# Kernel tuning notes

Hardware: AMD Instinct MI355X
Metric: run time of the kernel (lower is better)

## Reference

```python
import jax, jax.numpy as jnp
import numpy as np

B, T, C, H, W = 2, 8, 4, 128, 128
P = 8; D = 128; DEPTH = 2; E = 4; HD = 2 * D
Hp, Wp = H // P, W // P; F2 = 2 * D; CPP = C * P * P


def _ln(x, g, b):
    m = x.mean(-1, keepdims=True)
    v = ((x - m) ** 2).mean(-1, keepdims=True)
    return (x - m) * jax.lax.rsqrt(v + 1e-5) * g + b


def setup_inputs():
    key = jax.random.key(0)
    it = iter(jax.random.split(key, 32))
    def n(shape, s=0.02):
        return jax.random.normal(next(it), shape, jnp.float32) * s
    z = lambda shape: jnp.zeros(shape, jnp.float32)
    return {
        "x": jax.random.normal(next(it), (B, T, C, H, W), jnp.float32),
        "dt": jax.random.uniform(next(it), (T,), jnp.float32, 0.1, 1.0),
        "enc_Wre": n((CPP, D)), "enc_Wim": n((CPP, D)),
        "dec_W": n((F2, CPP)), "dec_b": z((CPP,)),
        "ln_sp_g": jnp.ones((DEPTH, F2), jnp.float32), "ln_sp_b": z((DEPTH, F2)),
        "conv_W": n((DEPTH, F2, F2, 3, 3), 0.05), "conv_b": z((DEPTH, F2)),
        "E_re": n((DEPTH, D, D), 0.05), "E_im": n((DEPTH, D, D), 0.05),
        "Dc_re": n((DEPTH, D, D), 0.05), "Dc_im": n((DEPTH, D, D), 0.05),
        "gate_W": n((DEPTH, F2, D)), "gate_b": z((DEPTH, D)),
        "src_W": n((DEPTH, F2, F2)), "src_b": z((DEPTH, F2)),
        "flux_decay": z((DEPTH, D)),
        "lam_re": n((DEPTH, D), 0.5), "lam_im": n((DEPTH, D), 0.5),
        "ln_t_g": jnp.ones((DEPTH, F2), jnp.float32), "ln_t_b": z((DEPTH, F2)),
        "rtr_W": n((DEPTH, F2, E)),
        "W1": n((DEPTH, E, F2, HD)), "b1": z((DEPTH, E, HD)),
        "W2": n((DEPTH, E, HD, F2)), "b2": z((DEPTH, E, F2)),
    }


def _forward(x, dt, enc_Wre, enc_Wim, dec_W, dec_b, ln_sp_g, ln_sp_b, conv_W, conv_b,
             E_re, E_im, Dc_re, Dc_im, gate_W, gate_b, src_W, src_b, flux_decay,
             lam_re, lam_im, ln_t_g, ln_t_b, rtr_W, W1, b1, W2, b2):
    Bx, Tx = x.shape[:2]
    # patch-embed encoder -> complex latent [B,T,D,Hp,Wp]
    f = x.reshape(Bx, Tx, C, Hp, P, Wp, P).transpose(0, 1, 3, 5, 2, 4, 6).reshape(Bx, Tx, Hp, Wp, CPP)
    zc = (f @ enc_Wre) + 1j * (f @ enc_Wim)
    zc = zc.transpose(0, 1, 4, 2, 3)
    dtBT = jnp.broadcast_to(dt[None, :], (Bx, Tx))
    flux = jnp.zeros((Bx, D), jnp.complex64)
    for i in range(DEPTH):
        # spatial branch: LayerNorm over [re,im] channels + Clifford-style 3x3 conv
        zr = jnp.concatenate([zc.real, zc.imag], axis=2).reshape(Bx * Tx, F2, Hp, Wp)
        xn = _ln(zr.transpose(0, 2, 3, 1), ln_sp_g[i], ln_sp_b[i]).transpose(0, 3, 1, 2)
        xs = jax.lax.conv_general_dilated(xn, conv_W[i], (1, 1), 'SAME',
                                          dimension_numbers=('NCHW', 'OIHW', 'NCHW')) + conv_b[i][None, :, None, None]
        sre, sim = jnp.split(xs, 2, axis=1)
        zc = zc + (sre + 1j * sim).reshape(Bx, Tx, D, Hp, Wp)
        # eigen-basis encode (complex channel mixing)
        xe = zc.transpose(0, 1, 3, 4, 2) @ (E_re[i] + 1j * E_im[i])  # B,T,Hp,Wp,D
        xm = xe.mean(axis=(2, 3))  # B,T,D complex
        # sequential flux tracker: inherently recurrent -> lax.scan over T
        gW, gb, sW, sb = gate_W[i], gate_b[i], src_W[i], src_b[i]
        dec = jax.nn.sigmoid(flux_decay[i])
        def step(fl, xmt):
            inp = jnp.concatenate([xmt.real, xmt.imag], -1)
            gate = jax.nn.sigmoid(inp @ gW + gb)
            s2 = inp @ sW + sb
            src = s2[..., :D] + 1j * s2[..., D:]
            fn = dec * fl + gate * xmt + (1.0 - gate) * src
            return fn, (fn, src)
        flux, (flux_seq, src_seq) = jax.lax.scan(step, flux, xm.transpose(1, 0, 2))
        flux_seq = flux_seq.transpose(1, 0, 2)
        src_seq = src_seq.transpose(1, 0, 2)
        g = jax.nn.sigmoid(jnp.concatenate([flux_seq.real, flux_seq.imag], -1) @ gW + gb)[:, :, None, None, :]
        forcing = xe * g + src_seq[:, :, None, None, :] * (1.0 - g)
        # complex transition operators (ZOH-style discretization)
        lam = -jax.nn.softplus(lam_re[i]) + 1j * lam_im[i]  # [D]
        opd = jnp.exp(dtBT[:, :, None] * lam[None, None, :])  # B,T,D complex
        opf = (opd - 1.0) / lam
        u = forcing * opf[:, :, None, None, :]
        A = jnp.broadcast_to(opd[:, :, None, None, :], u.shape)
        def comb(a, b):
            aA, aX = a
            bA, bX = b
            return (aA * bA, bX + bA * aX)
        # parallel pscan over time: h_t = A_t*h_{t-1} + u_t, independent per (B,Hp,Wp)
        _, uo = jax.lax.associative_scan(comb, (A, u), axis=1)
        xo = uo @ (Dc_re[i] + 1j * Dc_im[i])  # basis decode, B,T,Hp,Wp,D
        xon = _ln(jnp.concatenate([xo.real, xo.imag], -1), ln_t_g[i], ln_t_b[i])
        xcc = xon[..., :D] + 1j * xon[..., D:]
        # MoE FFN with soft routing over experts
        ft = jnp.concatenate([xcc.real, xcc.imag], -1).reshape(-1, F2)  # [M,2D]
        gates = jax.nn.softmax(ft @ rtr_W[i], axis=-1)  # [M,E]
        hmid = jax.nn.gelu(jnp.einsum('mf,efh->emh', ft, W1[i]) + b1[i][:, None, :])
        oexp = jnp.einsum('emh,ehf->emf', hmid, W2[i]) + b2[i][:, None, :]
        dtok = jnp.einsum('me,emf->mf', gates, oexp).reshape(Bx, Tx, Hp, Wp, F2)
        delta = dtok[..., :D] + 1j * dtok[..., D:]
        zc = zc + (xcc + delta).transpose(0, 1, 4, 2, 3)
    # decoder: project [re,im] -> pixels and unpatchify (real output)
    zl = zc.transpose(0, 1, 3, 4, 2)
    fo = jnp.concatenate([zl.real, zl.imag], -1) @ dec_W + dec_b
    return fo.reshape(Bx, Tx, Hp, Wp, C, P, P).transpose(0, 1, 4, 2, 5, 3, 6).reshape(Bx, Tx, C, H, W)


def reference(x, dt, enc_Wre, enc_Wim, dec_W, dec_b, ln_sp_g, ln_sp_b, conv_W, conv_b,
              E_re, E_im, Dc_re, Dc_im, gate_W, gate_b, src_W, src_b, flux_decay,
              lam_re, lam_im, ln_t_g, ln_t_b, rtr_W, W1, b1, W2, b2):
    return _forward(x, dt, enc_Wre, enc_Wim, dec_W, dec_b, ln_sp_g, ln_sp_b, conv_W, conv_b,
                    E_re, E_im, Dc_re, Dc_im, gate_W, gate_b, src_W, src_b, flux_decay,
                    lam_re, lam_im, ln_t_g, ln_t_b, rtr_W, W1, b1, W2, b2)
```

## Files before the change

kernel.cpp:

```cpp
#include <hip/hip_runtime.h>
#include <hip/hip_bf16.h>
#include <math.h>


#define NIN 28
typedef unsigned short u16;
typedef __attribute__((ext_vector_type(8))) short bf16x8;
typedef __attribute__((ext_vector_type(4))) float f32x4;
typedef __attribute__((ext_vector_type(8))) unsigned short us8;
typedef __attribute__((ext_vector_type(4))) unsigned short us4;

__device__ __forceinline__ float b2f(u16 u){ union{unsigned i;float f;}v; v.i=((unsigned)u)<<16; return v.f; }
__device__ __forceinline__ u16 f2b(float x){ __hip_bfloat16 h=__float2bfloat16(x); return *(u16*)&h; }
__device__ __forceinline__ float loadraw(const void* p, size_t i, int bf){
  return bf? b2f(((const u16*)p)[i]) : ((const float*)p)[i];
}
__device__ __forceinline__ float d_sigmoid(float x){ return 1.0f/(1.0f+expf(-x)); }
__device__ __forceinline__ float d_softplus(float x){ return fmaxf(x,0.0f)+log1pf(expf(-fabsf(x))); }
__device__ __forceinline__ float d_gelu(float x){
  const float c=0.7978845608028654f;
  return 0.5f*x*(1.0f+tanhf(c*(x+0.044715f*x*x*x)));
}

__global__ void detect_k(const void* lnspg, int* flag){
  unsigned w=*(const unsigned*)lnspg;
  *flag=(w==0x3F803F80u)?1:0;
}

#define NF32 17
struct MP {
  const void* src[NIN];
  int f32dst[NF32]; int f32cum[NF32+1];
  int seg[7];
};

__global__ __launch_bounds__(256) void mega_prep(MP a, const int* __restrict__ flag, float* __restrict__ W,
    u16* __restrict__ encB, u16* __restrict__ decB, u16* __restrict__ convB,
    u16* __restrict__ cplxB, u16* __restrict__ w1B, u16* __restrict__ w2c,
    const int* f32srcIdx_unused){
  int g=blockIdx.x*256+threadIdx.x;
  if(g>=a.seg[6]) return;
  int bf=*flag;
  if(g<a.seg[0]){
    int i=0;
    while(i<NF32-1 && g>=a.f32cum[i+1]) i++;
    int local=g-a.f32cum[i];
    const int needs[NF32]={1,5,6,7,9,14,15,16,17,18,19,20,21,22,23,25,27};
    W[a.f32dst[i]+local]=loadraw(a.src[needs[i]], local, bf);
  } else if(g<a.seg[1]){
    int idx=g-a.seg[0]; int n=idx>>8, k=idx&255;
    float v=(n<128)? loadraw(a.src[2],(size_t)k*128+n,bf) : loadraw(a.src[3],(size_t)k*128+(n-128),bf);
    encB[idx]=f2b(v);
  } else if(g<a.seg[2]){
    int idx=g-a.seg[1]; int n=idx>>8, k=idx&255;
    decB[idx]=f2b(loadraw(a.src[4],(size_t)k*256+n,bf));
  } else if(g<a.seg[3]){
    int idx=g-a.seg[2];
    int i=idx/589824; int r=idx-i*589824;
    int o=r/2304; int k=r-o*2304;
    int kg=k>>8, ic=k&255; int ky=kg/3, kx=kg-3*ky;
    size_t s=((((size_t)i*256+o)*256+ic)*3+ky)*3+kx;
    convB[idx]=f2b(loadraw(a.src[8],s,bf));
  } else if(g<a.seg[4]){
    int idx=g-a.seg[3];
    int mat=idx>>16; int r=idx&65535; int n=r>>8, k=r&255;
    int depth=mat&1; int isD=mat>>1;
    const void* re=isD? a.src[12]:a.src[10];
    const void* im=isD? a.src[13]:a.src[11];
    size_t base=(size_t)depth*16384;
    float v;
    if(k<128){ v = (n<128)? loadraw(re,base+(size_t)k*128+n,bf) : loadraw(im,base+(size_t)k*128+(n-128),bf); }
    else{ int kk=k-128;
      v = (n<128)? -loadraw(im,base+(size_t)kk*128+n,bf) : loadraw(re,base+(size_t)kk*128+(n-128),bf); }
    cplxB[idx]=f2b(v);
  } else if(g<a.seg[5]){
    int idx=g-a.seg[4]; int m=idx>>16; int r=idx&65535; int n=r>>8, k=r&255;
    w1B[idx]=f2b(loadraw(a.src[24],(size_t)m*65536+(size_t)k*256+n,bf));
  } else {
    int idx=g-a.seg[5];
    int i=idx>>18; int r=idx&262143; int n=r>>10; int k=r&1023;
    int e=k>>8, h=k&255;
    size_t s=(((size_t)(i*4+e)*256+h)*256+n);
    w2c[idx]=f2b(loadraw(a.src[26],s,bf));
  }
}

#define FB_BIAS 1
#define FB_GELU 2
#define FB_RS 4
#define FB_ADDTO 8
#define FB_WF32 16
#define FB_WBF16 32
#define FB_CONV 64
#define FB_GATHER 128
#define FB_MOE2 256
#define FB_UNPATCH 512

template<int FLAGS>
__global__ __launch_bounds__(512,2) void mfma_gemm(
    const void* __restrict__ Asrc, const u16* __restrict__ Bt,
    const float* __restrict__ bias, const float* __restrict__ gates,
    float* __restrict__ Cf, u16* __restrict__ Cb,
    const u16* __restrict__ Xtra, void* __restrict__ Cout, const int* __restrict__ flagp,
    int K, long aE, long bE, long biasE, long cE, long cRow)
{
  __shared__ u16 As[64][72];
  __shared__ u16 Bs[64][72];
  const int e=blockIdx.z;
  const u16* A=(const u16*)Asrc + (size_t)e*aE;
  Bt += (size_t)e*bE;
  const float* biasp = bias? bias+(size_t)e*biasE : nullptr;
  const int bn=blockIdx.x*64, bm=blockIdx.y*64;
  const int tid=threadIdx.x, l=tid&63, w=tid>>6;
  const int wm=w&3, wn=w>>2;
  const int row=tid>>3, col8=(tid&7)<<3;
  int bf=0;
  if(FLAGS&(FB_GATHER|FB_UNPATCH)) bf=*flagp;
  const us8 z8={0,0,0,0,0,0,0,0};
  us8 ra, rbv;

  auto loadA=[&](int k0){
    int gk=k0+col8;
    if(FLAGS&FB_CONV){
      int m=bm+row; int bt=m>>8, rem=m&255, hp=rem>>4, wp=rem&15;
      int kg=gk>>8, ic=gk&255; int ky=kg/3, kx=kg-3*ky;
      int y=hp+ky-1, x=wp+kx-1;
      ra = ((unsigned)y<16u && (unsigned)x<16u)?
           *(const us8*)&A[(((size_t)(bt*16+y))*16+x)*256+ic] : z8;
    } else if(FLAGS&FB_GATHER){
      int m=bm+row; int bt=m>>8, rem=m&255, hp=rem>>4, wp=rem&15;
      int c=gk>>6, ph=(gk>>3)&7;
      size_t sidx=(((size_t)bt*4+c)<<14)+(size_t)((hp*8+ph)<<7)+wp*8;
      if(bf) ra=*(const us8*)&((const u16*)Asrc)[sidx];
      else{
        const float* xf=(const float*)Asrc + sidx;
        us8 t;
        #pragma unroll
        for(int j=0;j<8;j++) t[j]=f2b(xf[j]);
        ra=t;
      }
    } else {
      ra=*(const us8*)&A[(size_t)(bm+row)*K+gk];
    }
  };
  auto loadB=[&](int k0){ rbv=*(const us8*)&Bt[(size_t)(bn+row)*K+k0+col8]; };

  loadA(0); loadB(0);
  f32x4 acc0={0.f,0.f,0.f,0.f}, acc1={0.f,0.f,0.f,0.f};
  const int kSteps=K>>6;
  for(int ks=0; ks<kSteps; ++ks){
    __syncthreads();
    *(us8*)&As[row][col8]=ra;
    *(us8*)&Bs[row][col8]=rbv;
    if(ks+1<kSteps){ loadA((ks+1)<<6); loadB((ks+1)<<6); }
    __syncthreads();
    #pragma unroll
    for(int kk=0;kk<64;kk+=32){
      const int kc=kk+((l>>4)<<3);
      bf16x8 a =*(const bf16x8*)&As[wm*16      +(l&15)][kc];
      bf16x8 b0=*(const bf16x8*)&Bs[wn*32      +(l&15)][kc];
      bf16x8 b1=*(const bf16x8*)&Bs[wn*32 + 16 +(l&15)][kc];
      acc0=__builtin_amdgcn_mfma_f32_16x16x32_bf16(a,b0,acc0,0,0,0);
      acc1=__builtin_amdgcn_mfma_f32_16x16x32_bf16(a,b1,acc1,0,0,0);
    }
  }

  const int rr=(l>>4)<<2, cc=l&15;
  #pragma unroll
  for(int ni=0;ni<2;ni++){
    f32x4 av = ni? acc1:acc0;
    #pragma unroll
    for(int r=0;r<4;r++){
      int m=bm+wm*16+rr+r;
      int n=bn+wn*32+ni*16+cc;
      float v=av[r];
      if(FLAGS&FB_BIAS) v+=biasp[n];
      if(FLAGS&FB_GELU) v=d_gelu(v);
      if(FLAGS&FB_RS)   v*=gates[(size_t)m*4+e];
      if(FLAGS&FB_MOE2){
        #pragma unroll
        for(int ee=0;ee<4;ee++) v+=gates[(size_t)m*4+ee]*bias[ee*256+n];
        v+=b2f(Xtra[(size_t)m*256+n]);
      }
      if(FLAGS&FB_UNPATCH){
        int bt=m>>8, hp=(m>>4)&15, wp=m&15;
        int c=n>>6, ph=(n>>3)&7, pw=n&7;
        size_t o=((size_t)bt<<16)|((size_t)c<<14)|((size_t)(hp*8+ph)<<7)|(size_t)(wp*8+pw);
        if(bf) ((__hip_bfloat16*)Cout)[o]=__float2bfloat16(v);
        else   ((float*)Cout)[o]=v;
        continue;
      }
      size_t o=(size_t)e*cE + (size_t)m*cRow + n;
      if(FLAGS&FB_ADDTO) v+=Cf[o];
      if(FLAGS&(FB_WF32|FB_ADDTO)) Cf[o]=v;
      if(FLAGS&FB_WBF16) Cb[o]=f2b(v);
    }
  }
}

__global__ __launch_bounds__(256) void ln4_k(const float* __restrict__ X,
    const float* __restrict__ g, const float* __restrict__ b, u16* __restrict__ out,
    const float* __restrict__ rtr, float* __restrict__ gates){
  int row=blockIdx.x*4+(threadIdx.x>>6);
  int l=threadIdx.x&63;
  f32x4 v=*(const f32x4*)&X[(size_t)row*256+l*4];
  float s=v[0]+v[1]+v[2]+v[3];
  #pragma unroll
  for(int o=32;o;o>>=1) s+=__shfl_xor(s,o);
  float mean=s*(1.0f/256.0f);
  float d0=v[0]-mean,d1=v[1]-mean,d2=v[2]-mean,d3=v[3]-mean;
  float q=d0*d0+d1*d1+d2*d2+d3*d3;
  #pragma unroll
  for(int o=32;o;o>>=1) q+=__shfl_xor(q,o);
  float rs=rsqrtf(q*(1.0f/256.0f)+1e-5f);
  float nv[4]={d0,d1,d2,d3};
  us4 o4;
  #pragma unroll
  for(int j=0;j<4;j++){ nv[j]=nv[j]*rs*g[l*4+j]+b[l*4+j]; o4[j]=f2b(nv[j]); }
  *(us4*)&out[(size_t)row*256+l*4]=o4;
  if(rtr){
    float p[4]={0.f,0.f,0.f,0.f};
    #pragma unroll
    for(int j=0;j<4;j++)
      #pragma unroll
      for(int ee=0;ee<4;ee++) p[ee]+=nv[j]*rtr[(l*4+j)*4+ee];
    #pragma unroll
    for(int ee=0;ee<4;ee++)
      #pragma unroll
      for(int o=32;o;o>>=1) p[ee]+=__shfl_xor(p[ee],o);
    if(l==0){
      float mx=fmaxf(fmaxf(p[0],p[1]),fmaxf(p[2],p[3]));
      float e0=expf(p[0]-mx),e1=expf(p[1]-mx),e2=expf(p[2]-mx),e3=expf(p[3]-mx);
      float inv=1.0f/(e0+e1+e2+e3);
      gates[row*4+0]=e0*inv; gates[row*4+1]=e1*inv; gates[row*4+2]=e2*inv; gates[row*4+3]=e3*inv;
    }
  }
}

__global__ __launch_bounds__(256) void reduce_xm4(const float* __restrict__ xe, float* __restrict__ xm4){
  int bt=blockIdx.x, ch=blockIdx.y, c=threadIdx.x;
  const float* base=xe+((size_t)bt*256+ch*64)*256+c;
  float s=0.f;
  #pragma unroll 4
  for(int sp=0;sp<64;sp++) s+=base[(size_t)sp*256];
  xm4[(bt*4+ch)*256+c]=s;
}

__global__ __launch_bounds__(384) void gate_src_k(const float* __restrict__ xm4,
    const float* __restrict__ sW, const float* __restrict__ sb,
    const float* __restrict__ gW, const float* __restrict__ gb,
    float* __restrict__ xm, float* __restrict__ s2, float* __restrict__ gt,
    const float* __restrict__ dt, const float* __restrict__ lam_re, const float* __restrict__ lam_im,
    float* __restrict__ odr_, float* __restrict__ odi_, float* __restrict__ ofr_, float* __restrict__ ofi_){
  int tid=threadIdx.x;
  if(blockIdx.x==16){
    for(int idx=tid; idx<1024; idx+=384){
      int t=idx>>7, d=idx&127;
      float lr=-d_softplus(lam_re[d]);
      float li=lam_im[d];
      float dtv=dt[t];
      float er=expf(dtv*lr);
      float odr=er*cosf(dtv*li), odi=er*sinf(dtv*li);
      float den=lr*lr+li*li;
      float ar=odr-1.0f, ai=odi;
      odr_[idx]=odr; odi_[idx]=odi;
      ofr_[idx]=(ar*lr+ai*li)/den;
      ofi_[idx]=(ai*lr-ar*li)/den;
    }
    return;
  }
  int bt=blockIdx.x;
  __shared__ float inp[256];
  if(tid<256){
    float v=(xm4[(bt*4+0)*256+tid]+xm4[(bt*4+1)*256+tid]
            +xm4[(bt*4+2)*256+tid]+xm4[(bt*4+3)*256+tid])*(1.0f/256.0f);
    inp[tid]=v; xm[bt*256+tid]=v;
  }
  __syncthreads();
  if(tid<256){
    float acc=sb[tid];
    for(int k=0;k<256;k++) acc+=inp[k]*sW[k*256+tid];
    s2[bt*256+tid]=acc;
  }else{
    int d=tid-256;
    float acc=gb[d];
    for(int k=0;k<256;k++) acc+=inp[k]*gW[k*128+d];
    gt[bt*128+d]=d_sigmoid(acc);
  }
}

__global__ __launch_bounds__(128) void flux_gate2(const float* __restrict__ xm,
    const float* __restrict__ s2, const float* __restrict__ gt,
    const float* __restrict__ fdec, const float* __restrict__ fbin, float* __restrict__ fbout,
    const float* __restrict__ gW, const float* __restrict__ gb, float* __restrict__ gbuf, int init){
  int bt=blockIdx.x; int b=bt>>3, t=bt&7; int d=threadIdx.x;
  float flr = init? 0.f : fbin[b*256+d];
  float fli = init? 0.f : fbin[b*256+128+d];
  float dec = d_sigmoid(fdec[d]);
  for(int tp=0; tp<=t; tp++){
    int q=b*8+tp;
    float gv=gt[q*128+d];
    flr = dec*flr + gv*xm[q*256+d]     + (1.0f-gv)*s2[q*256+d];
    fli = dec*fli + gv*xm[q*256+128+d] + (1.0f-gv)*s2[q*256+128+d];
  }
  __shared__ float inp[256];
  inp[d]=flr; inp[128+d]=fli;
  __syncthreads();
  float acc=gb[d];
  for(int k=0;k<256;k++) acc+=inp[k]*gW[k*128+d];
  gbuf[bt*128+d]=d_sigmoid(acc);
  if(t==7){ fbout[b*256+d]=flr; fbout[b*256+128+d]=fli; }
}

__global__ __launch_bounds__(256) void fscan_t(const float* __restrict__ xe,
    const float* __restrict__ gbuf, const float* __restrict__ ss,
    const float* __restrict__ odr, const float* __restrict__ odi,
    const float* __restrict__ ofr, const float* __restrict__ ofi, u16* __restrict__ uo){
  int idx=blockIdx.x*256+threadIdx.x;
  int d=idx&127, s=(idx>>7)&255, b=idx>>15;
  float hr=0.f, hi=0.f;
  for(int t=0;t<8;t++){
    int bt=b*8+t;
    size_t n=(size_t)bt*256+s;
    float g=gbuf[bt*128+d];
    float sr=ss[bt*256+d], si=ss[bt*256+128+d];
    float xr=xe[n*256+d], xi=xe[n*256+128+d];
    float fr=xr*g+sr*(1.0f-g), fi=xi*g+si*(1.0f-g);
    float pr=ofr[t*128+d], pi=ofi[t*128+d];
    float ur=fr*pr-fi*pi, ui=fr*pi+fi*pr;
    float ar=odr[t*128+d], ai=odi[t*128+d];
    float nr=ar*hr-ai*hi+ur, ni=ar*hi+ai*hr+ui;
    hr=nr; hi=ni;
    uo[n*256+d]=f2b(hr); uo[n*256+128+d]=f2b(hi);
  }
}

extern "C" void kernel_launch(void* const* d_in, const int* in_sizes, int n_in,
                              void* d_out, int out_size, void* d_ws, size_t ws_size,
                              hipStream_t stream){
  (void)out_size; (void)ws_size; (void)n_in;
  int acum[NIN+1]; acum[0]=0;
  for(int i=0;i<NIN;i++) acum[i+1]=acum[i]+((i==0)?0:in_sizes[i]);
  const int totalA=acum[NIN];
  float* W=(float*)d_ws;
  size_t off=((size_t)totalA+63)&~(size_t)63;
  int*   flag=(int*)(W+off); off+=64;
  float* zc  =W+off; off+=1048576;
  float* xe  =W+off; off+=1048576;
  u16* zcb =(u16*)(W+off); off+=524288;
  u16* xnb =(u16*)(W+off); off+=524288;
  u16* uob =(u16*)(W+off); off+=524288;
  u16* ftb =(u16*)(W+off); off+=524288;
  u16* hmid=(u16*)(W+off); off+=2097152;
  u16* encB=(u16*)(W+off); off+=32768;
  u16* decB=(u16*)(W+off); off+=32768;
  u16* convB=(u16*)(W+off); off+=589824;
  u16* cplxB=(u16*)(W+off); off+=131072;
  u16* w1B =(u16*)(W+off); off+=262144;
  u16* w2c =(u16*)(W+off); off+=262144;
  float* xm4 =W+off; off+=16384;
  float* xm  =W+off; off+=4096;
  float* s2  =W+off; off+=4096;
  float* gt  =W+off; off+=2048;
  float* gbuf=W+off; off+=2048;
  float* odr =W+off; off+=1024;
  float* odi =W+off; off+=1024;
  float* ofr =W+off; off+=1024;
  float* ofi =W+off; off+=1024;
  float* gates=W+off; off+=16384;
  float* fbA =W+off; off+=512;
  float* fbB =W+off; off+=512;

  detect_k<<<1,1,0,stream>>>(d_in[6], flag);

  MP mp;
  for(int i=0;i<NIN;i++) mp.src[i]=d_in[i];
  const int needs[NF32]={1,5,6,7,9,14,15,16,17,18,19,20,21,22,23,25,27};
  mp.f32cum[0]=0;
  for(int j=0;j<NF32;j++){ mp.f32cum[j+1]=mp.f32cum[j]+in_sizes[needs[j]]; mp.f32dst[j]=acum[needs[j]]; }
  int s0=mp.f32cum[NF32];
  mp.seg[0]=s0;
  mp.seg[1]=mp.seg[0]+65536;
  mp.seg[2]=mp.seg[1]+65536;
  mp.seg[3]=mp.seg[2]+1179648;
  mp.seg[4]=mp.seg[3]+262144;
  mp.seg[5]=mp.seg[4]+524288;
  mp.seg[6]=mp.seg[5]+524288;
  mega_prep<<<(mp.seg[6]+255)/256,256,0,stream>>>(mp, flag, W, encB, decB, convB, cplxB, w1B, w2c, nullptr);

  const dim3 GG(4,64,1);
  mfma_gemm<FB_GATHER|FB_WF32><<<GG,512,0,stream>>>(d_in[0], encB, nullptr, nullptr,
      zc, nullptr, nullptr, nullptr, flag, 256, 0,0,0,0,256);

  for(int i=0;i<2;i++){
    const float* lnspg=W+acum[6]+i*256;
    const float* lnspb=W+acum[7]+i*256;
    const float* convb=W+acum[9]+i*256;
    const float* gWp  =W+acum[14]+i*32768;
    const float* gbp  =W+acum[15]+i*128;
    const float* sWp  =W+acum[16]+i*65536;
    const float* sbp  =W+acum[17]+i*256;
    const float* fdec =W+acum[18]+i*128;
    const float* lamre=W+acum[19]+i*128;
    const float* lamim=W+acum[20]+i*128;
    const float* lntg =W+acum[21]+i*256;
    const float* lntb =W+acum[22]+i*256;
    const float* rtr  =W+acum[23]+i*1024;
    const float* b1   =W+acum[25]+i*1024;
    const float* b2   =W+acum[27]+i*1024;

    ln4_k<<<1024,256,0,stream>>>(zc, lnspg, lnspb, xnb, nullptr, nullptr);
    mfma_gemm<FB_CONV|FB_BIAS|FB_ADDTO|FB_WBF16><<<GG,512,0,stream>>>(xnb, convB+(size_t)i*589824,
        convb, nullptr, zc, zcb, nullptr, nullptr, nullptr, 2304, 0,0,0,0,256);
    mfma_gemm<FB_WF32><<<GG,512,0,stream>>>(zcb, cplxB+(size_t)i*65536, nullptr, nullptr,
        xe, nullptr, nullptr, nullptr, nullptr, 256, 0,0,0,0,256);
    reduce_xm4<<<dim3(16,4),256,0,stream>>>(xe, xm4);
    gate_src_k<<<17,384,0,stream>>>(xm4, sWp, sbp, gWp, gbp, xm, s2, gt,
        W+acum[1], lamre, lamim, odr, odi, ofr, ofi);
    flux_gate2<<<16,128,0,stream>>>(xm, s2, gt, fdec, (i==0)?nullptr:fbA, (i==0)?fbA:fbB,
        gWp, gbp, gbuf, (i==0)?1:0);
    fscan_t<<<256,256,0,stream>>>(xe, gbuf, s2, odr, odi, ofr, ofi, uob);
    mfma_gemm<FB_WF32><<<GG,512,0,stream>>>(uob, cplxB+(size_t)(2+i)*65536, nullptr, nullptr,
        xe, nullptr, nullptr, nullptr, nullptr, 256, 0,0,0,0,256);
    ln4_k<<<1024,256,0,stream>>>(xe, lntg, lntb, ftb, rtr, gates);
    mfma_gemm<FB_BIAS|FB_GELU|FB_RS|FB_WBF16><<<dim3(4,64,4),512,0,stream>>>(ftb, w1B+(size_t)i*262144,
        b1, gates, nullptr, hmid, nullptr, nullptr, nullptr, 256, 0,65536,256,256,1024);
    mfma_gemm<FB_MOE2|FB_ADDTO|FB_WBF16><<<GG,512,0,stream>>>(hmid, w2c+(size_t)i*262144,
        b2, gates, zc, zcb, ftb, nullptr, nullptr, 1024, 0,0,0,0,256);
  }

  mfma_gemm<FB_BIAS|FB_UNPATCH><<<GG,512,0,stream>>>(zcb, decB, W+acum[5], nullptr,
      nullptr, nullptr, nullptr, d_out, flag, 256, 0,0,0,0,256);
}
```

Baseline: 211.9 us.

## Fuse spatial-mean reduction into GEMM epilogue, merge flux kernels, load B from global

The spatial mean reduction (reduce_xm4) is folded into the epilogue of the complex-mixing GEMM, which writes per-block column sums via a small LDS reduction. gate_src_k and flux_gate2 are merged into one flux_all kernel that recomputes src/gate projections per timestep inside the scan. The GEMM stops staging B tiles in LDS and has each wave load its B fragments straight from global memory with register double-buffering. Together these cut kernel launches and LDS traffic. In exchange, B loads go uncoalesced and duplicated across waves, and flux_all does redundant matvecs for earlier timesteps on only 16 blocks.

```diff
diff --git a/kernel.cpp b/kernel.cpp
--- a/kernel.cpp
+++ b/kernel.cpp
@@ -36,8 +36,7 @@
 
 __global__ __launch_bounds__(256) void mega_prep(MP a, const int* __restrict__ flag, float* __restrict__ W,
     u16* __restrict__ encB, u16* __restrict__ decB, u16* __restrict__ convB,
-    u16* __restrict__ cplxB, u16* __restrict__ w1B, u16* __restrict__ w2c,
-    const int* f32srcIdx_unused){
+    u16* __restrict__ cplxB, u16* __restrict__ w1B, u16* __restrict__ w2c){
   int g=blockIdx.x*256+threadIdx.x;
   if(g>=a.seg[6]) return;
   int bf=*flag;
@@ -95,6 +94,7 @@
 #define FB_GATHER 128
 #define FB_MOE2 256
 #define FB_UNPATCH 512
+#define FB_XM 1024
 
 template<int FLAGS>
 __global__ __launch_bounds__(512,2) void mfma_gemm(
@@ -102,10 +102,10 @@
     const float* __restrict__ bias, const float* __restrict__ gates,
     float* __restrict__ Cf, u16* __restrict__ Cb,
     const u16* __restrict__ Xtra, void* __restrict__ Cout, const int* __restrict__ flagp,
-    int K, long aE, long bE, long biasE, long cE, long cRow)
+    int K, long aE, long bE, long biasE, long cE, long cRow,
+    float* __restrict__ xm4)
 {
   __shared__ u16 As[64][72];
-  __shared__ u16 Bs[64][72];
   const int e=blockIdx.z;
   const u16* A=(const u16*)Asrc + (size_t)e*aE;
   Bt += (size_t)e*bE;
@@ -117,7 +117,7 @@
   int bf=0;
   if(FLAGS&(FB_GATHER|FB_UNPATCH)) bf=*flagp;
   const us8 z8={0,0,0,0,0,0,0,0};
-  us8 ra, rbv;
+  us8 ra;
 
   auto loadA=[&](int k0){
     int gk=k0+col8;
@@ -143,26 +143,38 @@
       ra=*(const us8*)&A[(size_t)(bm+row)*K+gk];
     }
   };
-  auto loadB=[&](int k0){ rbv=*(const us8*)&Bt[(size_t)(bn+row)*K+k0+col8]; };
-
-  loadA(0); loadB(0);
+  const int bRow0 = bn + wn*32 + (l&15);
+  const int bColL = (l>>4)<<3;
+  auto loadBf=[&](int k0, int kk, int ni)->us8{
+    return *(const us8*)&Bt[(size_t)(bRow0+ni*16)*K + k0 + kk + bColL];
+  };
+
+  loadA(0);
+  us8 c00=loadBf(0,0,0), c01=loadBf(0,0,1), c10=loadBf(0,32,0), c11=loadBf(0,32,1);
+
   f32x4 acc0={0.f,0.f,0.f,0.f}, acc1={0.f,0.f,0.f,0.f};
   const int kSteps=K>>6;
   for(int ks=0; ks<kSteps; ++ks){
     __syncthreads();
     *(us8*)&As[row][col8]=ra;
-    *(us8*)&Bs[row][col8]=rbv;
-    if(ks+1<kSteps){ loadA((ks+1)<<6); loadB((ks+1)<<6); }
-    __syncthreads();
-    #pragma unroll
-    for(int kk=0;kk<64;kk+=32){
-      const int kc=kk+((l>>4)<<3);
-      bf16x8 a =*(const bf16x8*)&As[wm*16      +(l&15)][kc];
-      bf16x8 b0=*(const bf16x8*)&Bs[wn*32      +(l&15)][kc];
-      bf16x8 b1=*(const bf16x8*)&Bs[wn*32 + 16 +(l&15)][kc];
-      acc0=__builtin_amdgcn_mfma_f32_16x16x32_bf16(a,b0,acc0,0,0,0);
-      acc1=__builtin_amdgcn_mfma_f32_16x16x32_bf16(a,b1,acc1,0,0,0);
-    }
+    const bool more = (ks+1<kSteps);
+    if(more) loadA((ks+1)<<6);
+    __syncthreads();
+    us8 n00,n01,n10,n11;
+    if(more){
+      int k0=(ks+1)<<6;
+      n00=loadBf(k0,0,0); n01=loadBf(k0,0,1); n10=loadBf(k0,32,0); n11=loadBf(k0,32,1);
+    }
+    {
+      const int kc0 = (l>>4)<<3;
+      bf16x8 a0=*(const bf16x8*)&As[wm*16+(l&15)][kc0];
+      bf16x8 a1=*(const bf16x8*)&As[wm*16+(l&15)][32+kc0];
+      acc0=__builtin_amdgcn_mfma_f32_16x16x32_bf16(a0,*(bf16x8*)&c00,acc0,0,0,0);
+      acc1=__builtin_amdgcn_mfma_f32_16x16x32_bf16(a0,*(bf16x8*)&c01,acc1,0,0,0);
+      acc0=__builtin_amdgcn_mfma_f32_16x16x32_bf16(a1,*(bf16x8*)&c10,acc0,0,0,0);
+      acc1=__builtin_amdgcn_mfma_f32_16x16x32_bf16(a1,*(bf16x8*)&c11,acc1,0,0,0);
+    }
+    if(more){ c00=n00; c01=n01; c10=n10; c11=n11; }
   }
 
   const int rr=(l>>4)<<2, cc=l&15;
@@ -194,6 +206,24 @@
       if(FLAGS&FB_ADDTO) v+=Cf[o];
       if(FLAGS&(FB_WF32|FB_ADDTO)) Cf[o]=v;
       if(FLAGS&FB_WBF16) Cb[o]=f2b(v);
+    }
+  }
+
+  if(FLAGS&FB_XM){
+    float cs0=acc0[0]+acc0[1]+acc0[2]+acc0[3];
+    float cs1=acc1[0]+acc1[1]+acc1[2]+acc1[3];
+    cs0+=__shfl_xor(cs0,16); cs0+=__shfl_xor(cs0,32);
+    cs1+=__shfl_xor(cs1,16); cs1+=__shfl_xor(cs1,32);
+    __syncthreads();
+    float* xr=(float*)&As[0][0];
+    if(l<16){
+      xr[wm*64 + wn*32 + cc]      = cs0;
+      xr[wm*64 + wn*32 + 16 + cc] = cs1;
+    }
+    __syncthreads();
+    if(tid<64){
+      float s=xr[tid]+xr[64+tid]+xr[128+tid]+xr[192+tid];
+      xm4[(size_t)blockIdx.y*256 + bn + tid]=s;
     }
   }
 }
@@ -237,21 +267,14 @@
   }
 }
 
-__global__ __launch_bounds__(256) void reduce_xm4(const float* __restrict__ xe, float* __restrict__ xm4){
-  int bt=blockIdx.x, ch=blockIdx.y, c=threadIdx.x;
-  const float* base=xe+((size_t)bt*256+ch*64)*256+c;
-  float s=0.f;
-  #pragma unroll 4
-  for(int sp=0;sp<64;sp++) s+=base[(size_t)sp*256];
-  xm4[(bt*4+ch)*256+c]=s;
-}
-
-__global__ __launch_bounds__(384) void gate_src_k(const float* __restrict__ xm4,
+__global__ __launch_bounds__(384) void flux_all(const float* __restrict__ xm4,
     const float* __restrict__ sW, const float* __restrict__ sb,
     const float* __restrict__ gW, const float* __restrict__ gb,
-    float* __restrict__ xm, float* __restrict__ s2, float* __restrict__ gt,
+    const float* __restrict__ fdec, const float* __restrict__ fbin, float* __restrict__ fbout,
+    float* __restrict__ s2out, float* __restrict__ gbuf,
     const float* __restrict__ dt, const float* __restrict__ lam_re, const float* __restrict__ lam_im,
-    float* __restrict__ odr_, float* __restrict__ odi_, float* __restrict__ ofr_, float* __restrict__ ofi_){
+    float* __restrict__ odr_, float* __restrict__ odi_, float* __restrict__ ofr_, float* __restrict__ ofi_,
+    int init){
   int tid=threadIdx.x;
   if(blockIdx.x==16){
     for(int idx=tid; idx<1024; idx+=384){
@@ -269,47 +292,44 @@
     }
     return;
   }
-  int bt=blockIdx.x;
-  __shared__ float inp[256];
-  if(tid<256){
-    float v=(xm4[(bt*4+0)*256+tid]+xm4[(bt*4+1)*256+tid]
-            +xm4[(bt*4+2)*256+tid]+xm4[(bt*4+3)*256+tid])*(1.0f/256.0f);
-    inp[tid]=v; xm[bt*256+tid]=v;
-  }
+  int bt=blockIdx.x, b=bt>>3, t=bt&7;
+  __shared__ float xms[8][256];
+  __shared__ float s2s[256], gts[128], fl[256];
+  for(int idx=tid; idx<(t+1)*256; idx+=384){
+    int tp=idx>>8, c=idx&255;
+    int rb=(b*8+tp)*4;
+    xms[tp][c]=(xm4[(size_t)rb*256+c]+xm4[(size_t)(rb+1)*256+c]
+               +xm4[(size_t)(rb+2)*256+c]+xm4[(size_t)(rb+3)*256+c])*(1.0f/256.0f);
+  }
+  if(tid<256) fl[tid]= init? 0.f : fbin[b*256+tid];
   __syncthreads();
-  if(tid<256){
-    float acc=sb[tid];
-    for(int k=0;k<256;k++) acc+=inp[k]*sW[k*256+tid];
-    s2[bt*256+tid]=acc;
-  }else{
-    int d=tid-256;
-    float acc=gb[d];
-    for(int k=0;k<256;k++) acc+=inp[k]*gW[k*128+d];
-    gt[bt*128+d]=d_sigmoid(acc);
-  }
-}
-
-__global__ __launch_bounds__(128) void flux_gate2(const float* __restrict__ xm,
-    const float* __restrict__ s2, const float* __restrict__ gt,
-    const float* __restrict__ fdec, const float* __restrict__ fbin, float* __restrict__ fbout,
-    const float* __restrict__ gW, const float* __restrict__ gb, float* __restrict__ gbuf, int init){
-  int bt=blockIdx.x; int b=bt>>3, t=bt&7; int d=threadIdx.x;
-  float flr = init? 0.f : fbin[b*256+d];
-  float fli = init? 0.f : fbin[b*256+128+d];
-  float dec = d_sigmoid(fdec[d]);
   for(int tp=0; tp<=t; tp++){
-    int q=b*8+tp;
-    float gv=gt[q*128+d];
-    flr = dec*flr + gv*xm[q*256+d]     + (1.0f-gv)*s2[q*256+d];
-    fli = dec*fli + gv*xm[q*256+128+d] + (1.0f-gv)*s2[q*256+128+d];
-  }
-  __shared__ float inp[256];
-  inp[d]=flr; inp[128+d]=fli;
-  __syncthreads();
-  float acc=gb[d];
-  for(int k=0;k<256;k++) acc+=inp[k]*gW[k*128+d];
-  gbuf[bt*128+d]=d_sigmoid(acc);
-  if(t==7){ fbout[b*256+d]=flr; fbout[b*256+128+d]=fli; }
+    if(tid<256){
+      float acc=sb[tid];
+      for(int k=0;k<256;k++) acc+=xms[tp][k]*sW[k*256+tid];
+      s2s[tid]=acc;
+    }else{
+      int d=tid-256;
+      float acc=gb[d];
+      for(int k=0;k<256;k++) acc+=xms[tp][k]*gW[k*128+d];
+      gts[d]=d_sigmoid(acc);
+    }
+    __syncthreads();
+    if(tid<256){
+      int d=tid&127;
+      float dec=d_sigmoid(fdec[d]);
+      float gv=gts[d];
+      fl[tid]=dec*fl[tid]+gv*xms[tp][tid]+(1.0f-gv)*s2s[tid];
+    }
+    __syncthreads();
+  }
+  if(tid<256) s2out[bt*256+tid]=s2s[tid];
+  if(tid<128){
+    float acc=gb[tid];
+    for(int k=0;k<256;k++) acc+=fl[k]*gW[k*128+tid];
+    gbuf[bt*128+tid]=d_sigmoid(acc);
+  }
+  if(t==7 && tid<256) fbout[b*256+tid]=fl[tid];
 }
 
 __global__ __launch_bounds__(256) void fscan_t(const float* __restrict__ xe,
@@ -359,9 +379,7 @@
   u16* w1B =(u16*)(W+off); off+=262144;
   u16* w2c =(u16*)(W+off); off+=262144;
   float* xm4 =W+off; off+=16384;
-  float* xm  =W+off; off+=4096;
   float* s2  =W+off; off+=4096;
-  float* gt  =W+off; off+=2048;
   float* gbuf=W+off; off+=2048;
   float* odr =W+off; off+=1024;
   float* odi =W+off; off+=1024;
@@ -378,19 +396,18 @@
   const int needs[NF32]={1,5,6,7,9,14,15,16,17,18,19,20,21,22,23,25,27};
   mp.f32cum[0]=0;
   for(int j=0;j<NF32;j++){ mp.f32cum[j+1]=mp.f32cum[j]+in_sizes[needs[j]]; mp.f32dst[j]=acum[needs[j]]; }
-  int s0=mp.f32cum[NF32];
-  mp.seg[0]=s0;
+  mp.seg[0]=mp.f32cum[NF32];
   mp.seg[1]=mp.seg[0]+65536;
   mp.seg[2]=mp.seg[1]+65536;
   mp.seg[3]=mp.seg[2]+1179648;
   mp.seg[4]=mp.seg[3]+262144;
   mp.seg[5]=mp.seg[4]+524288;
   mp.seg[6]=mp.seg[5]+524288;
-  mega_prep<<<(mp.seg[6]+255)/256,256,0,stream>>>(mp, flag, W, encB, decB, convB, cplxB, w1B, w2c, nullptr);
+  mega_prep<<<(mp.seg[6]+255)/256,256,0,stream>>>(mp, flag, W, encB, decB, convB, cplxB, w1B, w2c);
 
   const dim3 GG(4,64,1);
   mfma_gemm<FB_GATHER|FB_WF32><<<GG,512,0,stream>>>(d_in[0], encB, nullptr, nullptr,
-      zc, nullptr, nullptr, nullptr, flag, 256, 0,0,0,0,256);
+      zc, nullptr, nullptr, nullptr, flag, 256, 0,0,0,0,256, nullptr);
 
   for(int i=0;i<2;i++){
     const float* lnspg=W+acum[6]+i*256;
@@ -411,24 +428,22 @@
 
     ln4_k<<<1024,256,0,stream>>>(zc, lnspg, lnspb, xnb, nullptr, nullptr);
     mfma_gemm<FB_CONV|FB_BIAS|FB_ADDTO|FB_WBF16><<<GG,512,0,stream>>>(xnb, convB+(size_t)i*589824,
-        convb, nullptr, zc, zcb, nullptr, nullptr, nullptr, 2304, 0,0,0,0,256);
-    mfma_gemm<FB_WF32><<<GG,512,0,stream>>>(zcb, cplxB+(size_t)i*65536, nullptr, nullptr,
-        xe, nullptr, nullptr, nullptr, nullptr, 256, 0,0,0,0,256);
-    reduce_xm4<<<dim3(16,4),256,0,stream>>>(xe, xm4);
-    gate_src_k<<<17,384,0,stream>>>(xm4, sWp, sbp, gWp, gbp, xm, s2, gt,
-        W+acum[1], lamre, lamim, odr, odi, ofr, ofi);
-    flux_gate2<<<16,128,0,stream>>>(xm, s2, gt, fdec, (i==0)?nullptr:fbA, (i==0)?fbA:fbB,
-        gWp, gbp, gbuf, (i==0)?1:0);
+        convb, nullptr, zc, zcb, nullptr, nullptr, nullptr, 2304, 0,0,0,0,256, nullptr);
+    mfma_gemm<FB_WF32|FB_XM><<<GG,512,0,stream>>>(zcb, cplxB+(size_t)i*65536, nullptr, nullptr,
+        xe, nullptr, nullptr, nullptr, nullptr, 256, 0,0,0,0,256, xm4);
+    flux_all<<<17,384,0,stream>>>(xm4, sWp, sbp, gWp, gbp, fdec,
+        (i==0)?nullptr:fbA, (i==0)?fbA:fbB, s2, gbuf,
+        W+acum[1], lamre, lamim, odr, odi, ofr, ofi, (i==0)?1:0);
     fscan_t<<<256,256,0,stream>>>(xe, gbuf, s2, odr, odi, ofr, ofi, uob);
     mfma_gemm<FB_WF32><<<GG,512,0,stream>>>(uob, cplxB+(size_t)(2+i)*65536, nullptr, nullptr,
-        xe, nullptr, nullptr, nullptr, nullptr, 256, 0,0,0,0,256);
+        xe, nullptr, nullptr, nullptr, nullptr, 256, 0,0,0,0,256, nullptr);
     ln4_k<<<1024,256,0,stream>>>(xe, lntg, lntb, ftb, rtr, gates);
     mfma_gemm<FB_BIAS|FB_GELU|FB_RS|FB_WBF16><<<dim3(4,64,4),512,0,stream>>>(ftb, w1B+(size_t)i*262144,
-        b1, gates, nullptr, hmid, nullptr, nullptr, nullptr, 256, 0,65536,256,256,1024);
+        b1, gates, nullptr, hmid, nullptr, nullptr, nullptr, 256, 0,65536,256,256,1024, nullptr);
     mfma_gemm<FB_MOE2|FB_ADDTO|FB_WBF16><<<GG,512,0,stream>>>(hmid, w2c+(size_t)i*262144,
-        b2, gates, zc, zcb, ftb, nullptr, nullptr, 1024, 0,0,0,0,256);
+        b2, gates, zc, zcb, ftb, nullptr, nullptr, 1024, 0,0,0,0,256, nullptr);
   }
 
   mfma_gemm<FB_BIAS|FB_UNPATCH><<<GG,512,0,stream>>>(zcb, decB, W+acum[5], nullptr,
-      nullptr, nullptr, nullptr, d_out, flag, 256, 0,0,0,0,256);
-}
+      nullptr, nullptr, nullptr, d_out, flag, 256, 0,0,0,0,256, nullptr);
+}
```

New measurement: 403.1 us. +90.2%, slower.
